# Kernel tuning notes

Measured on AMD Instinct MI355X. Metric: run time of the kernel, lower is better.

## Reference

```python
import jax, jax.numpy as jnp
import numpy as np
from jax import lax

B, L, NCH, NQ, NL, FW, NCLS = 256, 3000, 4, 8, 2, 128, 5
BN_EPS = 1e-5


def setup_inputs() -> dict:
    key = jax.random.key(0)
    ks = jax.random.split(key, 24)
    rn = lambda k, shape, s=0.05: jax.random.normal(k, shape, jnp.float32) * s
    inp = {}
    inp['x'] = jax.random.normal(ks[0], (B, NCH, L), jnp.float32)
    inp['conv1_w'] = rn(ks[1], (32, NCH, 7)); inp['conv1_b'] = rn(ks[2], (32,))
    inp['bn1_g'] = 1.0 + rn(ks[3], (32,)); inp['bn1_b'] = rn(ks[3], (32,))
    inp['conv2_w'] = rn(ks[4], (64, 32, 7)); inp['conv2_b'] = rn(ks[5], (64,))
    inp['bn2_g'] = 1.0 + rn(ks[6], (64,)); inp['bn2_b'] = rn(ks[6], (64,))
    inp['conv3_w'] = rn(ks[7], (128, 64, 7)); inp['conv3_b'] = rn(ks[8], (128,))
    inp['bn3_g'] = 1.0 + rn(ks[9], (128,)); inp['bn3_b'] = rn(ks[9], (128,))
    inp['conv4_w'] = rn(ks[10], (128, 128, 7)); inp['conv4_b'] = rn(ks[11], (128,))
    inp['bn4_g'] = 1.0 + rn(ks[12], (128,)); inp['bn4_b'] = rn(ks[12], (128,))
    inp['fc_w'] = rn(ks[13], (FW, 128)); inp['fc_b'] = rn(ks[14], (FW,))
    inp['ang_w'] = rn(ks[15], (NQ, FW)); inp['ang_b'] = rn(ks[16], (NQ,))
    # TorchLayer default init: uniform in [0, 2*pi)
    inp['qw'] = jax.random.uniform(ks[17], (NL, NQ, 3), jnp.float32, 0.0, 2.0 * np.pi)
    inp['h1_w'] = rn(ks[18], (64, NQ)); inp['h1_b'] = rn(ks[19], (64,))
    inp['h2_w'] = rn(ks[20], (NCLS, 64)); inp['h2_b'] = rn(ks[21], (NCLS,))
    return inp


def _conv1d(x, w, b):
    y = lax.conv_general_dilated(x, w, (1,), [(3, 3)], dimension_numbers=('NCH', 'OIH', 'NCH'))
    return y + b[None, :, None]


def _bn(x, g, b):  # eval-mode BN: running_mean=0, running_var=1
    inv = 1.0 / np.sqrt(1.0 + BN_EPS)
    return x * (g * inv)[None, :, None] + b[None, :, None]


def _maxpool4(x):
    return lax.reduce_window(x, -jnp.inf, lax.max, (1, 1, 4), (1, 1, 4), 'VALID')


def _apply_1q(state, U, w, batched):
    # state: (B, 2**NQ); wire 0 = most significant bit (PennyLane convention)
    bs = state.shape[0]
    st = state.reshape(bs, 2 ** w, 2, -1)
    if batched:
        new = jnp.einsum('sab,slbr->slar', U, st)
    else:
        new = jnp.einsum('ab,slbr->slar', U, st)
    return new.reshape(bs, -1)


def _apply_cnot(state, c, t):
    bs = state.shape[0]
    q1, q2 = min(c, t), max(c, t)
    s = state.reshape(bs, 2 ** q1, 2, 2 ** (q2 - q1 - 1), 2, -1)
    ci, ti = (2, 4) if c < t else (4, 2)
    c0 = lax.index_in_dim(s, 0, ci, keepdims=True)
    c1 = jnp.flip(lax.index_in_dim(s, 1, ci, keepdims=True), axis=ti)
    return jnp.concatenate([c0, c1], axis=ci).reshape(bs, -1)


def _rot_matrix(phi, th, om):
    # PennyLane Rot(phi, theta, omega) = RZ(omega) RY(theta) RZ(phi)
    cm, sm = jnp.cos(th / 2), jnp.sin(th / 2)
    m00 = jnp.exp(-0.5j * (phi + om)) * cm
    m01 = -jnp.exp(0.5j * (phi - om)) * sm
    m10 = jnp.exp(-0.5j * (phi - om)) * sm
    m11 = jnp.exp(0.5j * (phi + om)) * cm
    return jnp.stack([jnp.stack([m00, m01]), jnp.stack([m10, m11])]).astype(jnp.complex64)


def _qsim(angles, qw):
    bs = angles.shape[0]
    dim = 2 ** NQ
    state = jnp.zeros((bs, dim), jnp.complex64).at[:, 0].set(1.0)
    # AngleEmbedding: RY(angle_w) on each wire (batched matrices)
    c, s = jnp.cos(angles / 2), jnp.sin(angles / 2)
    for w in range(NQ):
        U = jnp.stack([jnp.stack([c[:, w], -s[:, w]], -1),
                       jnp.stack([s[:, w], c[:, w]], -1)], -2).astype(jnp.complex64)
        state = _apply_1q(state, U, w, batched=True)
    # StronglyEntanglingLayers: Rot on each wire, then CNOT ring with range r
    for l in range(NL):
        for w in range(NQ):
            U = _rot_matrix(qw[l, w, 0], qw[l, w, 1], qw[l, w, 2])
            state = _apply_1q(state, U, w, batched=False)
        r = (l % (NQ - 1)) + 1
        for i in range(NQ):
            state = _apply_cnot(state, i, (i + r) % NQ)
    probs = state.real ** 2 + state.imag ** 2
    z = [probs.reshape(bs, 2 ** w, 2, -1)[:, :, 0].sum((1, 2))
         - probs.reshape(bs, 2 ** w, 2, -1)[:, :, 1].sum((1, 2)) for w in range(NQ)]
    return jnp.stack(z, -1)  # (B, NQ)


def reference(x, conv1_w, conv1_b, bn1_g, bn1_b, conv2_w, conv2_b, bn2_g, bn2_b,
              conv3_w, conv3_b, bn3_g, bn3_b, conv4_w, conv4_b, bn4_g, bn4_b,
              fc_w, fc_b, ang_w, ang_b, qw, h1_w, h1_b, h2_w, h2_b):
    h = jax.nn.relu(_bn(_conv1d(x, conv1_w, conv1_b), bn1_g, bn1_b))
    h = jax.nn.relu(_bn(_conv1d(h, conv2_w, conv2_b), bn2_g, bn2_b))
    h = _maxpool4(h)
    h = jax.nn.relu(_bn(_conv1d(h, conv3_w, conv3_b), bn3_g, bn3_b))
    h = _maxpool4(h)
    h = jax.nn.relu(_bn(_conv1d(h, conv4_w, conv4_b), bn4_g, bn4_b))
    h = h.mean(-1)  # AdaptiveAvgPool1d(1) + Flatten -> (B, 128)
    h = jax.nn.relu(h @ fc_w.T + fc_b)  # Dropout is identity in eval
    raw = h @ ang_w.T + ang_b
    angles = np.pi * jnp.tanh(raw)
    q = _qsim(angles, qw)
    h2 = jax.nn.relu(q @ h1_w.T + h1_b)
    return h2 @ h2_w.T + h2_b
```

## Files before the change

### kernel.cpp

```cpp
#include <hip/hip_runtime.h>
#include <hip/hip_bf16.h>

#define BN_INV 0.9999950000375f
#define PI_F   3.14159265358979f

typedef __attribute__((ext_vector_type(8))) short s16x8;
typedef __attribute__((ext_vector_type(4))) float f32x4;
typedef __attribute__((ext_vector_type(4))) unsigned short u16x4;

__device__ inline unsigned short f2bf(float f) {
  union { float f; unsigned u; } v; v.f = f;
  unsigned r = v.u + 0x7fffu + ((v.u >> 16) & 1u);
  return (unsigned short)(r >> 16);
}

__global__ __launch_bounds__(256) void k_pack(
    const float* __restrict__ w1, const float* __restrict__ w2,
    const float* __restrict__ w3, const float* __restrict__ w4,
    unsigned short* __restrict__ w1p, unsigned short* __restrict__ w2p,
    unsigned short* __restrict__ w3p, unsigned short* __restrict__ w4p,
    float* __restrict__ h4)
{
  int e = blockIdx.x * 256 + threadIdx.x;
  if (e < 2048) {
    int co = e >> 6, k = e & 63, kk = k >> 3, ci = k & 7;
    w1p[e] = (ci < 4 && kk < 7) ? f2bf(w1[co * 28 + ci * 7 + kk]) : (unsigned short)0;
  } else if (e < 16384) {
    int t = e - 2048; int co = t / 224, k = t % 224, kk = k >> 5, ci = k & 31;
    w2p[t] = f2bf(w2[co * 224 + ci * 7 + kk]);
  } else if (e < 73728) {
    int t = e - 16384; int co = t / 448, k = t % 448, kk = k >> 6, ci = k & 63;
    w3p[t] = f2bf(w3[co * 448 + ci * 7 + kk]);
  } else if (e < 188416) {
    int t = e - 73728; int co = t / 896, k = t % 896, kk = k >> 7, ci = k & 127;
    w4p[t] = f2bf(w4[co * 896 + ci * 7 + kk]);
  } else if (e < 221184) {
    h4[e - 188416] = 0.f;
  }
}

__global__ __launch_bounds__(256) void k_conv1(
    const float* __restrict__ x, const unsigned short* __restrict__ w1p,
    const float* __restrict__ cb, const float* __restrict__ bng,
    const float* __restrict__ bnb, unsigned short* __restrict__ h1t)
{
  __shared__ __align__(16) char lds[520 * 16 + 4096 + 256];
  float* scs = (float*)(lds + 520 * 16 + 4096);
  const int tid = threadIdx.x;
  const int b = blockIdx.y;
  const int l0 = blockIdx.x * 512;

  for (int r = tid; r < 519; r += 256) {
    int gr = l0 + r - 3;
    s16x8 v;
    if (gr >= 0 && gr < 3000) {
      const float* xr = x + b * 4 * 3000 + gr;
      v[0] = (short)f2bf(xr[0]);
      v[1] = (short)f2bf(xr[3000]);
      v[2] = (short)f2bf(xr[6000]);
      v[3] = (short)f2bf(xr[9000]);
      v[4] = 0; v[5] = 0; v[6] = 0; v[7] = 0;
    } else {
      for (int i = 0; i < 8; ++i) v[i] = 0;
    }
    *(s16x8*)(lds + r * 16) = v;
  }
  {
    int co = tid >> 3, c = tid & 7;
    s16x8 v = *(const s16x8*)(w1p + co * 64 + c * 8);
    *(s16x8*)(lds + 8320 + ((co * 128 + c * 16) ^ ((co & 7) << 4))) = v;
  }
  if (tid < 32) {
    float sc = bng[tid] * BN_INV;
    scs[tid * 2] = sc;
    scs[tid * 2 + 1] = fmaf(cb[tid], sc, bnb[tid]);
  }
  __syncthreads();

  const int w = tid >> 6, l = tid & 63, lr = l & 15, g = l >> 4;
  const int wp = w * 128;
  f32x4 acc[2][8];
  for (int m = 0; m < 2; ++m)
    for (int n = 0; n < 8; ++n)
      for (int i = 0; i < 4; ++i) acc[m][n][i] = 0.f;

  #pragma unroll
  for (int s = 0; s < 2; ++s) {
    s16x8 a[2], bf[8];
    #pragma unroll
    for (int m = 0; m < 2; ++m) {
      int co = m * 16 + lr;
      a[m] = *(const s16x8*)(lds + 8320 + ((co * 128 + s * 64 + g * 16) ^ ((co & 7) << 4)));
    }
    #pragma unroll
    for (int n = 0; n < 8; ++n) {
      int row = wp + n * 16 + lr + s * 4 + g;
      bf[n] = *(const s16x8*)(lds + row * 16);
    }
    #pragma unroll
    for (int m = 0; m < 2; ++m)
      #pragma unroll
      for (int n = 0; n < 8; ++n)
        acc[m][n] = __builtin_amdgcn_mfma_f32_16x16x32_bf16(a[m], bf[n], acc[m][n], 0, 0, 0);
  }

  #pragma unroll
  for (int m = 0; m < 2; ++m) {
    int co0 = m * 16 + g * 4;
    float sc[4], sh[4];
    #pragma unroll
    for (int j = 0; j < 4; ++j) { sc[j] = scs[(co0 + j) * 2]; sh[j] = scs[(co0 + j) * 2 + 1]; }
    #pragma unroll
    for (int n = 0; n < 8; ++n) {
      int gp = l0 + wp + n * 16 + lr;
      if (gp < 3000) {
        u16x4 o;
        #pragma unroll
        for (int j = 0; j < 4; ++j)
          o[j] = f2bf(fmaxf(fmaf(acc[m][n][j], sc[j], sh[j]), 0.f));
        *(u16x4*)(h1t + (b * 3000 + gp) * 32 + co0) = o;
      }
    }
  }
}

__global__ __launch_bounds__(256) void k_conv2(
    const unsigned short* __restrict__ h1t, const unsigned short* __restrict__ w2p,
    const float* __restrict__ cb, const float* __restrict__ bng,
    const float* __restrict__ bnb, unsigned short* __restrict__ h2pt)
{
  __shared__ __align__(16) char lds[46080];
  float* scs = (float*)(lds + 45568);
  const int tid = threadIdx.x, b = blockIdx.y;
  const int l0 = blockIdx.x * 256;

  for (int e = tid; e < 1048; e += 256) {
    int r = e >> 2, c = e & 3;
    int gr = l0 + r - 3;
    s16x8 v;
    if (gr >= 0 && gr < 3000) v = *(const s16x8*)(h1t + (b * 3000 + gr) * 32 + c * 8);
    else for (int i = 0; i < 8; ++i) v[i] = 0;
    *(s16x8*)(lds + ((r * 64 + c * 16) ^ ((r & 7) << 4))) = v;
  }
  for (int e = tid; e < 1792; e += 256) {
    int co = e / 28, c = e % 28;
    s16x8 v = *(const s16x8*)(w2p + co * 224 + c * 8);
    *(s16x8*)(lds + 16896 + ((co * 448 + c * 16) ^ ((co & 7) << 4))) = v;
  }
  if (tid < 64) {
    float sc = bng[tid] * BN_INV;
    scs[tid * 2] = sc;
    scs[tid * 2 + 1] = fmaf(cb[tid], sc, bnb[tid]);
  }
  __syncthreads();

  const int w = tid >> 6, l = tid & 63, lr = l & 15, g = l >> 4;
  const int wp = w * 64;
  f32x4 acc[4][4];
  for (int m = 0; m < 4; ++m)
    for (int n = 0; n < 4; ++n)
      for (int i = 0; i < 4; ++i) acc[m][n][i] = 0.f;

  #pragma unroll
  for (int s = 0; s < 7; ++s) {
    s16x8 xa[4], wb[4];
    #pragma unroll
    for (int m = 0; m < 4; ++m) {
      int row = wp + m * 16 + lr + s;
      xa[m] = *(const s16x8*)(lds + ((row * 64 + g * 16) ^ ((row & 7) << 4)));
    }
    #pragma unroll
    for (int n = 0; n < 4; ++n) {
      int co = n * 16 + lr;
      wb[n] = *(const s16x8*)(lds + 16896 + ((co * 448 + s * 64 + g * 16) ^ ((co & 7) << 4)));
    }
    #pragma unroll
    for (int m = 0; m < 4; ++m)
      #pragma unroll
      for (int n = 0; n < 4; ++n)
        acc[m][n] = __builtin_amdgcn_mfma_f32_16x16x32_bf16(xa[m], wb[n], acc[m][n], 0, 0, 0);
  }

  float sc[4], sh[4];
  #pragma unroll
  for (int n = 0; n < 4; ++n) {
    sc[n] = scs[(n * 16 + lr) * 2];
    sh[n] = scs[(n * 16 + lr) * 2 + 1];
  }
  #pragma unroll
  for (int m = 0; m < 4; ++m) {
    int pp = (l0 + wp + m * 16 + g * 4) >> 2;
    if (pp < 750) {
      unsigned short* orow = h2pt + (b * 750 + pp) * 64 + lr;
      #pragma unroll
      for (int n = 0; n < 4; ++n) {
        float v = fmaxf(fmaxf(acc[m][n][0], acc[m][n][1]),
                        fmaxf(acc[m][n][2], acc[m][n][3]));
        orow[n * 16] = f2bf(fmaxf(fmaf(v, sc[n], sh[n]), 0.f));
      }
    }
  }
}

__global__ __launch_bounds__(256) void k_conv3(
    const unsigned short* __restrict__ h2pt, const unsigned short* __restrict__ w3p,
    const float* __restrict__ cb, const float* __restrict__ bng,
    const float* __restrict__ bnb, unsigned short* __restrict__ h3pt)
{
  __shared__ __align__(16) char lds[75776];
  float* scs = (float*)(lds + 74752);
  const int tid = threadIdx.x, b = blockIdx.y;
  const int tile = blockIdx.x >> 1, ch = blockIdx.x & 1;
  const int l0 = tile * 128, cg0 = ch * 64;

  for (int e = tid; e < 1072; e += 256) {
    int r = e >> 3, c = e & 7;
    int gr = l0 + r - 3;
    s16x8 v;
    if (gr >= 0 && gr < 750) v = *(const s16x8*)(h2pt + (b * 750 + gr) * 64 + c * 8);
    else for (int i = 0; i < 8; ++i) v[i] = 0;
    *(s16x8*)(lds + ((r * 128 + c * 16) ^ ((r & 7) << 4))) = v;
  }
  for (int e = tid; e < 3584; e += 256) {
    int co = e / 56, c = e % 56;
    s16x8 v = *(const s16x8*)(w3p + (cg0 + co) * 448 + c * 8);
    *(s16x8*)(lds + 17408 + ((co * 896 + c * 16) ^ ((co & 7) << 4))) = v;
  }
  if (tid < 64) {
    int co = cg0 + tid;
    float sc = bng[co] * BN_INV;
    scs[tid * 2] = sc;
    scs[tid * 2 + 1] = fmaf(cb[co], sc, bnb[co]);
  }
  __syncthreads();

  const int w = tid >> 6, l = tid & 63, lr = l & 15, g = l >> 4;
  const int wp = w * 32;
  f32x4 acc[2][4];
  for (int m = 0; m < 2; ++m)
    for (int n = 0; n < 4; ++n)
      for (int i = 0; i < 4; ++i) acc[m][n][i] = 0.f;

  #pragma unroll
  for (int sl = 0; sl < 14; ++sl) {
    int kk = sl >> 1, cib = (sl & 1) * 32;
    s16x8 xa[2], wb[4];
    #pragma unroll
    for (int m = 0; m < 2; ++m) {
      int row = wp + m * 16 + lr + kk;
      xa[m] = *(const s16x8*)(lds + ((row * 128 + cib * 2 + g * 16) ^ ((row & 7) << 4)));
    }
    #pragma unroll
    for (int n = 0; n < 4; ++n) {
      int co = n * 16 + lr;
      wb[n] = *(const s16x8*)(lds + 17408 + ((co * 896 + sl * 64 + g * 16) ^ ((co & 7) << 4)));
    }
    #pragma unroll
    for (int m = 0; m < 2; ++m)
      #pragma unroll
      for (int n = 0; n < 4; ++n)
        acc[m][n] = __builtin_amdgcn_mfma_f32_16x16x32_bf16(xa[m], wb[n], acc[m][n], 0, 0, 0);
  }

  float sc[4], sh[4];
  #pragma unroll
  for (int n = 0; n < 4; ++n) {
    sc[n] = scs[(n * 16 + lr) * 2];
    sh[n] = scs[(n * 16 + lr) * 2 + 1];
  }
  #pragma unroll
  for (int m = 0; m < 2; ++m) {
    int pp = (l0 + wp + m * 16 + g * 4) >> 2;
    if (pp < 187) {
      unsigned short* orow = h3pt + (b * 187 + pp) * 128 + cg0 + lr;
      #pragma unroll
      for (int n = 0; n < 4; ++n) {
        float v = fmaxf(fmaxf(acc[m][n][0], acc[m][n][1]),
                        fmaxf(acc[m][n][2], acc[m][n][3]));
        orow[n * 16] = f2bf(fmaxf(fmaf(v, sc[n], sh[n]), 0.f));
      }
    }
  }
}

__global__ __launch_bounds__(256) void k_conv4(
    const unsigned short* __restrict__ h3pt, const unsigned short* __restrict__ w4p,
    const float* __restrict__ cb, const float* __restrict__ bng,
    const float* __restrict__ bnb, float* __restrict__ h4)
{
  __shared__ __align__(16) char lds[79872];
  float* scs = (float*)(lds + 79360);
  const int tid = threadIdx.x, b = blockIdx.y, ch = blockIdx.x;
  const int cg0 = ch * 64;

  #pragma unroll
  for (int i = 0; i < 13; ++i) {
    int e = tid + i * 256;
    if (e < 3168) {
      int r = e >> 4, c = e & 15, gr = r - 3;
      s16x8 v;
      if (gr >= 0 && gr < 187) v = *(const s16x8*)(h3pt + (b * 187 + gr) * 128 + c * 8);
      else for (int q = 0; q < 8; ++q) v[q] = 0;
      *(s16x8*)(lds + ((r * 256 + c * 16) ^ ((r & 7) << 4))) = v;
    }
  }
  for (int e = tid; e < 1792; e += 256) {
    int co = e / 28, c = e % 28;
    s16x8 v = *(const s16x8*)(w4p + (cg0 + co) * 896 + c * 8);
    *(s16x8*)(lds + 50688 + ((co * 448 + c * 16) ^ ((co & 7) << 4))) = v;
  }
  if (tid < 64) {
    int co = cg0 + tid;
    float sc = bng[co] * BN_INV;
    scs[tid * 2] = sc;
    scs[tid * 2 + 1] = fmaf(cb[co], sc, bnb[co]);
  }
  __syncthreads();

  const int w = tid >> 6, l = tid & 63, lr = l & 15, g = l >> 4;
  const int wp = w * 48;

  f32x4 acc[3][4];
  for (int m = 0; m < 3; ++m)
    for (int n = 0; n < 4; ++n)
      for (int i = 0; i < 4; ++i) acc[m][n][i] = 0.f;

  for (int chunk = 0; chunk < 4; ++chunk) {
    s16x8 wr[7];
    if (chunk < 3) {
      #pragma unroll
      for (int i = 0; i < 7; ++i) {
        int e = tid + i * 256;
        int co = e / 28, c = e % 28;
        wr[i] = *(const s16x8*)(w4p + (cg0 + co) * 896 + (chunk + 1) * 224 + c * 8);
      }
    }
    #pragma unroll
    for (int sl = 0; sl < 7; ++sl) {
      int k0 = chunk * 224 + sl * 32;
      int kk = k0 >> 7, cib = k0 & 127;
      s16x8 xa[3], wb[4];
      #pragma unroll
      for (int m = 0; m < 3; ++m) {
        int row = wp + m * 16 + lr + kk;
        xa[m] = *(const s16x8*)(lds + ((row * 256 + cib * 2 + g * 16) ^ ((row & 7) << 4)));
      }
      #pragma unroll
      for (int n = 0; n < 4; ++n) {
        int co = n * 16 + lr;
        wb[n] = *(const s16x8*)(lds + 50688 + ((co * 448 + sl * 64 + g * 16) ^ ((co & 7) << 4)));
      }
      #pragma unroll
      for (int m = 0; m < 3; ++m)
        #pragma unroll
        for (int n = 0; n < 4; ++n)
          acc[m][n] = __builtin_amdgcn_mfma_f32_16x16x32_bf16(xa[m], wb[n], acc[m][n], 0, 0, 0);
    }
    __syncthreads();
    if (chunk < 3) {
      #pragma unroll
      for (int i = 0; i < 7; ++i) {
        int e = tid + i * 256;
        int co = e / 28, c = e % 28;
        *(s16x8*)(lds + 50688 + ((co * 448 + c * 16) ^ ((co & 7) << 4))) = wr[i];
      }
    }
    __syncthreads();
  }

  float sc[4], sh[4];
  #pragma unroll
  for (int n = 0; n < 4; ++n) {
    sc[n] = scs[(n * 16 + lr) * 2];
    sh[n] = scs[(n * 16 + lr) * 2 + 1];
  }
  float psum[4] = {0.f, 0.f, 0.f, 0.f};
  #pragma unroll
  for (int m = 0; m < 3; ++m) {
    #pragma unroll
    for (int j = 0; j < 4; ++j) {
      int pos = wp + m * 16 + g * 4 + j;
      if (pos < 187) {
        #pragma unroll
        for (int n = 0; n < 4; ++n)
          psum[n] += fmaxf(fmaf(acc[m][n][j], sc[n], sh[n]), 0.f);
      }
    }
  }
  #pragma unroll
  for (int n = 0; n < 4; ++n) {
    float v = psum[n];
    v += __shfl_xor(v, 16);
    v += __shfl_xor(v, 32);
    if (l < 16)
      atomicAdd(&h4[b * 128 + cg0 + n * 16 + lr], v);
  }
}

__global__ __launch_bounds__(64) void k_head(
    const float* __restrict__ h4, const float* __restrict__ fc_w,
    const float* __restrict__ fc_b, const float* __restrict__ ang_w,
    const float* __restrict__ ang_b, const float* __restrict__ qw,
    const float* __restrict__ h1_w, const float* __restrict__ h1_b,
    const float* __restrict__ h2_w, const float* __restrict__ h2_b,
    float* __restrict__ out)
{
  const int lane = threadIdx.x;
  const int b = blockIdx.x;

  float hv0 = h4[b * 128 + lane] * (1.0f / 187.0f);
  float hv1 = h4[b * 128 + 64 + lane] * (1.0f / 187.0f);

  float a0 = fc_b[lane], a1 = fc_b[lane + 64];
  {
    const float* w0 = fc_w + lane * 128;
    const float* w1 = fc_w + (lane + 64) * 128;
    #pragma unroll
    for (int k = 0; k < 64; ++k) {
      float hk = __shfl(hv0, k);
      a0 = fmaf(hk, w0[k], a0);
      a1 = fmaf(hk, w1[k], a1);
    }
    #pragma unroll
    for (int k = 0; k < 64; ++k) {
      float hk = __shfl(hv1, k);
      a0 = fmaf(hk, w0[64 + k], a0);
      a1 = fmaf(hk, w1[64 + k], a1);
    }
  }
  float f0 = fmaxf(a0, 0.f), f1 = fmaxf(a1, 0.f);

  float rcw[8], rsw[8];
  #pragma unroll
  for (int o = 0; o < 8; ++o) {
    float p = fmaf(f0, ang_w[o * 128 + lane], f1 * ang_w[o * 128 + 64 + lane]);
    #pragma unroll
    for (int m = 1; m < 64; m <<= 1) p += __shfl_xor(p, m);
    float aa = PI_F * tanhf(ang_b[o] + p);
    rcw[o] = cosf(0.5f * aa);
    rsw[o] = sinf(0.5f * aa);
  }

  float r0, r1, r2, r3, r4, r5, r6, r7;
  {
    int gq = lane & 15;
    float phi = qw[gq * 3], th = qw[gq * 3 + 1], om = qw[gq * 3 + 2];
    float cm = cosf(0.5f * th), sm = sinf(0.5f * th);
    float ap = 0.5f * (phi + om), bm = 0.5f * (phi - om);
    float ca = cosf(ap), sa = sinf(ap), cb2 = cosf(bm), sb2 = sinf(bm);
    r0 = cm * ca;   r1 = -cm * sa;
    r2 = -sm * cb2; r3 = -sm * sb2;
    r4 = sm * cb2;  r5 = -sm * sb2;
    r6 = cm * ca;   r7 = cm * sa;
  }

  float2 st[4];
  st[0] = make_float2((lane == 0) ? 1.f : 0.f, 0.f);
  st[1] = make_float2(0.f, 0.f);
  st[2] = make_float2(0.f, 0.f);
  st[3] = make_float2(0.f, 0.f);

  auto ry_lane = [&](int lx, float c, float s) {
    #pragma unroll
    for (int j = 0; j < 4; ++j) {
      float ox = __shfl_xor(st[j].x, lx);
      float oy = __shfl_xor(st[j].y, lx);
      bool hi = (lane & lx) != 0;
      float a0x = hi ? ox : st[j].x, a0y = hi ? oy : st[j].y;
      float a1x = hi ? st[j].x : ox, a1y = hi ? st[j].y : oy;
      float cA = hi ? s : c, cB = hi ? c : -s;
      st[j].x = cA * a0x + cB * a1x;
      st[j].y = cA * a0y + cB * a1y;
    }
  };
#define RY_SLOT(J0, J1, c, s) { \
    float2 A = st[J0], B = st[J1]; \
    st[J0].x = (c) * A.x - (s) * B.x; st[J0].y = (c) * A.y - (s) * B.y; \
    st[J1].x = (s) * A.x + (c) * B.x; st[J1].y = (s) * A.y + (c) * B.y; }

  ry_lane(32, rcw[0], rsw[0]);
  ry_lane(16, rcw[1], rsw[1]);
  ry_lane(8,  rcw[2], rsw[2]);
  ry_lane(4,  rcw[3], rsw[3]);
  ry_lane(2,  rcw[4], rsw[4]);
  ry_lane(1,  rcw[5], rsw[5]);
  RY_SLOT(0, 2, rcw[6], rsw[6]); RY_SLOT(1, 3, rcw[6], rsw[6]);
  RY_SLOT(0, 1, rcw[7], rsw[7]); RY_SLOT(2, 3, rcw[7], rsw[7]);

  auto rot_lane = [&](int gi, int lx) {
    float m00x = __shfl(r0, gi), m00y = __shfl(r1, gi);
    float m01x = __shfl(r2, gi), m01y = __shfl(r3, gi);
    float m10x = __shfl(r4, gi), m10y = __shfl(r5, gi);
    float m11x = __shfl(r6, gi), m11y = __shfl(r7, gi);
    #pragma unroll
    for (int j = 0; j < 4; ++j) {
      float ox = __shfl_xor(st[j].x, lx);
      float oy = __shfl_xor(st[j].y, lx);
      bool hi = (lane & lx) != 0;
      float a0x = hi ? ox : st[j].x, a0y = hi ? oy : st[j].y;
      float a1x = hi ? st[j].x : ox, a1y = hi ? st[j].y : oy;
      float cx = hi ? m10x : m00x, cy = hi ? m10y : m00y;
      float dx = hi ? m11x : m01x, dy = hi ? m11y : m01y;
      st[j].x = cx * a0x - cy * a0y + dx * a1x - dy * a1y;
      st[j].y = cx * a0y + cy * a0x + dx * a1y + dy * a1x;
    }
  };
#define ROT_SLOT(J0, J1) { \
    float2 A = st[J0], B = st[J1]; \
    st[J0].x = m00x * A.x - m00y * A.y + m01x * B.x - m01y * B.y; \
    st[J0].y = m00x * A.y + m00y * A.x + m01x * B.y + m01y * B.x; \
    st[J1].x = m10x * A.x - m10y * A.y + m11x * B.x - m11y * B.y; \
    st[J1].y = m10x * A.y + m10y * A.x + m11x * B.y + m11y * B.x; }
  auto rot_slot = [&](int gi, int bit) {
    float m00x = __shfl(r0, gi), m00y = __shfl(r1, gi);
    float m01x = __shfl(r2, gi), m01y = __shfl(r3, gi);
    float m10x = __shfl(r4, gi), m10y = __shfl(r5, gi);
    float m11x = __shfl(r6, gi), m11y = __shfl(r7, gi);
    if (bit == 1) { ROT_SLOT(0, 2) ROT_SLOT(1, 3) }
    else          { ROT_SLOT(0, 1) ROT_SLOT(2, 3) }
  };

  auto cnot = [&](int cmask, int tmask) {
    bool cb0, cb1, cb2, cb3;
    if (cmask >= 4) {
      bool cbl = (lane & (cmask >> 2)) != 0;
      cb0 = cbl; cb1 = cbl; cb2 = cbl; cb3 = cbl;
    } else {
      cb0 = false;
      cb1 = (1 & cmask) != 0;
      cb2 = (2 & cmask) != 0;
      cb3 = (3 & cmask) != 0;
    }
    if (tmask >= 4) {
      int lx = tmask >> 2;
      { float ox = __shfl_xor(st[0].x, lx), oy = __shfl_xor(st[0].y, lx); if (cb0) { st[0].x = ox; st[0].y = oy; } }
      { float ox = __shfl_xor(st[1].x, lx), oy = __shfl_xor(st[1].y, lx); if (cb1) { st[1].x = ox; st[1].y = oy; } }
      { float ox = __shfl_xor(st[2].x, lx), oy = __shfl_xor(st[2].y, lx); if (cb2) { st[2].x = ox; st[2].y = oy; } }
      { float ox = __shfl_xor(st[3].x, lx), oy = __shfl_xor(st[3].y, lx); if (cb3) { st[3].x = ox; st[3].y = oy; } }
    } else {
      float2 o0 = st[0], o1 = st[1], o2 = st[2], o3 = st[3];
      if (tmask == 2) {
        if (cb0) st[0] = o2;
        if (cb1) st[1] = o3;
        if (cb2) st[2] = o0;
        if (cb3) st[3] = o1;
      } else {
        if (cb0) st[0] = o1;
        if (cb1) st[1] = o0;
        if (cb2) st[2] = o3;
        if (cb3) st[3] = o2;
      }
    }
  };

  #pragma unroll
  for (int lay = 0; lay < 2; ++lay) {
    rot_lane(lay * 8 + 0, 32);
    rot_lane(lay * 8 + 1, 16);
    rot_lane(lay * 8 + 2, 8);
    rot_lane(lay * 8 + 3, 4);
    rot_lane(lay * 8 + 4, 2);
    rot_lane(lay * 8 + 5, 1);
    rot_slot(lay * 8 + 6, 1);
    rot_slot(lay * 8 + 7, 0);
    int r = lay + 1;
    #pragma unroll
    for (int i = 0; i < 8; ++i) {
      int c = i, t = (i + r) & 7;
      cnot(1 << (7 - c), 1 << (7 - t));
    }
  }

  float p0 = st[0].x * st[0].x + st[0].y * st[0].y;
  float p1 = st[1].x * st[1].x + st[1].y * st[1].y;
  float p2 = st[2].x * st[2].x + st[2].y * st[2].y;
  float p3 = st[3].x * st[3].x + st[3].y * st[3].y;
  float sAll = p0 + p1 + p2 + p3;
  float zp[8];
  zp[0] = (lane & 32) ? -sAll : sAll;
  zp[1] = (lane & 16) ? -sAll : sAll;
  zp[2] = (lane & 8)  ? -sAll : sAll;
  zp[3] = (lane & 4)  ? -sAll : sAll;
  zp[4] = (lane & 2)  ? -sAll : sAll;
  zp[5] = (lane & 1)  ? -sAll : sAll;
  zp[6] = (p0 + p1) - (p2 + p3);
  zp[7] = (p0 - p1) + (p2 - p3);
  #pragma unroll
  for (int o = 0; o < 8; ++o) {
    #pragma unroll
    for (int m = 1; m < 64; m <<= 1) zp[o] += __shfl_xor(zp[o], m);
  }

  float ah = h1_b[lane];
  const float* hw = h1_w + lane * 8;
  #pragma unroll
  for (int k = 0; k < 8; ++k) ah = fmaf(zp[k], hw[k], ah);
  float hh = fmaxf(ah, 0.f);

  #pragma unroll
  for (int o = 0; o < 5; ++o) {
    float v = hh * h2_w[o * 64 + lane];
    #pragma unroll
    for (int m = 1; m < 64; m <<= 1) v += __shfl_xor(v, m);
    if (lane == 0) out[b * 5 + o] = v + h2_b[o];
  }
#undef RY_SLOT
#undef ROT_SLOT
}

extern "C" void kernel_launch(void* const* d_in, const int* in_sizes, int n_in,
                              void* d_out, int out_size, void* d_ws, size_t ws_size,
                              hipStream_t stream) {
  (void)in_sizes; (void)n_in; (void)out_size; (void)ws_size;
  const float* x    = (const float*)d_in[0];
  const float* c1w  = (const float*)d_in[1];
  const float* c1b  = (const float*)d_in[2];
  const float* b1g  = (const float*)d_in[3];
  const float* b1b  = (const float*)d_in[4];
  const float* c2w  = (const float*)d_in[5];
  const float* c2b  = (const float*)d_in[6];
  const float* b2g  = (const float*)d_in[7];
  const float* b2b  = (const float*)d_in[8];
  const float* c3w  = (const float*)d_in[9];
  const float* c3b  = (const float*)d_in[10];
  const float* b3g  = (const float*)d_in[11];
  const float* b3b  = (const float*)d_in[12];
  const float* c4w  = (const float*)d_in[13];
  const float* c4b  = (const float*)d_in[14];
  const float* b4g  = (const float*)d_in[15];
  const float* b4b  = (const float*)d_in[16];
  const float* fcw  = (const float*)d_in[17];
  const float* fcb  = (const float*)d_in[18];
  const float* angw = (const float*)d_in[19];
  const float* angb = (const float*)d_in[20];
  const float* qw   = (const float*)d_in[21];
  const float* h1w  = (const float*)d_in[22];
  const float* h1b  = (const float*)d_in[23];
  const float* h2w  = (const float*)d_in[24];
  const float* h2b  = (const float*)d_in[25];

  char* wsb = (char*)d_ws;
  unsigned short* w1p  = (unsigned short*)(wsb + 0);
  unsigned short* w2p  = (unsigned short*)(wsb + 4096);
  unsigned short* w3p  = (unsigned short*)(wsb + 32768);
  unsigned short* w4p  = (unsigned short*)(wsb + 147456);
  float*          h4   = (float*)(wsb + 393216);
  unsigned short* h1t  = (unsigned short*)(wsb + 1048576);
  unsigned short* h2pt = (unsigned short*)(wsb + 52428800);
  unsigned short* h3pt = (unsigned short*)(wsb + 79691776);

  k_pack<<<dim3(864), 256, 0, stream>>>(c1w, c2w, c3w, c4w, w1p, w2p, w3p, w4p, h4);
  k_conv1<<<dim3(6, 256),  256, 0, stream>>>(x, w1p, c1b, b1g, b1b, h1t);
  k_conv2<<<dim3(12, 256), 256, 0, stream>>>(h1t, w2p, c2b, b2g, b2b, h2pt);
  k_conv3<<<dim3(12, 256), 256, 0, stream>>>(h2pt, w3p, c3b, b3g, b3b, h3pt);
  k_conv4<<<dim3(2, 256),  256, 0, stream>>>(h3pt, w4p, c4b, b4g, b4b, h4);
  k_head<<<dim3(256), 64, 0, stream>>>(h4, fcw, fcb, angw, angb, qw,
                                       h1w, h1b, h2w, h2b, (float*)d_out);
}
```

Measured before the change: 229.6 us.

## Precompute quantum circuit unitary, batch head, and widen conv3 tiles

Adds a kernel that builds the full 256x256 complex unitary of the fixed variational circuit from qw. The head then applies it to the product-state input, which is formed from per-sample RY cos/sin products, with a small matrix-vector product per sample instead of simulating gates per sample. The head also processes four samples per block and uses a transposed fc weight that the pack kernel prepares. Separately, conv3 now computes all 128 output channels per block over a 128-position tile, double-staging weights through registers, which halves the grid and avoids loading the input tile twice; the larger accumulator raises register pressure.

```diff
diff --git a/kernel.cpp b/kernel.cpp
--- a/kernel.cpp
+++ b/kernel.cpp
@@ -17,9 +17,10 @@
 __global__ __launch_bounds__(256) void k_pack(
     const float* __restrict__ w1, const float* __restrict__ w2,
     const float* __restrict__ w3, const float* __restrict__ w4,
+    const float* __restrict__ fcw,
     unsigned short* __restrict__ w1p, unsigned short* __restrict__ w2p,
     unsigned short* __restrict__ w3p, unsigned short* __restrict__ w4p,
-    float* __restrict__ h4)
+    float* __restrict__ fcwt, float* __restrict__ h4)
 {
   int e = blockIdx.x * 256 + threadIdx.x;
   if (e < 2048) {
@@ -36,6 +37,9 @@
     w4p[t] = f2bf(w4[co * 896 + ci * 7 + kk]);
   } else if (e < 221184) {
     h4[e - 188416] = 0.f;
+  } else if (e < 237568) {
+    int t = e - 221184; int k = t >> 7, o = t & 127;
+    fcwt[t] = fcw[o * 128 + k];
   }
 }
 
@@ -210,8 +214,7 @@
   __shared__ __align__(16) char lds[75776];
   float* scs = (float*)(lds + 74752);
   const int tid = threadIdx.x, b = blockIdx.y;
-  const int tile = blockIdx.x >> 1, ch = blockIdx.x & 1;
-  const int l0 = tile * 128, cg0 = ch * 64;
+  const int l0 = blockIdx.x * 128;
 
   for (int e = tid; e < 1072; e += 256) {
     int r = e >> 3, c = e & 7;
@@ -222,62 +225,86 @@
     *(s16x8*)(lds + ((r * 128 + c * 16) ^ ((r & 7) << 4))) = v;
   }
   for (int e = tid; e < 3584; e += 256) {
-    int co = e / 56, c = e % 56;
-    s16x8 v = *(const s16x8*)(w3p + (cg0 + co) * 448 + c * 8);
-    *(s16x8*)(lds + 17408 + ((co * 896 + c * 16) ^ ((co & 7) << 4))) = v;
-  }
-  if (tid < 64) {
-    int co = cg0 + tid;
-    float sc = bng[co] * BN_INV;
+    int co = e / 28, c = e % 28;
+    s16x8 v = *(const s16x8*)(w3p + co * 448 + c * 8);
+    *(s16x8*)(lds + 17408 + ((co * 448 + c * 16) ^ ((co & 7) << 4))) = v;
+  }
+  if (tid < 128) {
+    float sc = bng[tid] * BN_INV;
     scs[tid * 2] = sc;
-    scs[tid * 2 + 1] = fmaf(cb[co], sc, bnb[co]);
-  }
-  __syncthreads();
-
-  const int w = tid >> 6, l = tid & 63, lr = l & 15, g = l >> 4;
-  const int wp = w * 32;
-  f32x4 acc[2][4];
-  for (int m = 0; m < 2; ++m)
+    scs[tid * 2 + 1] = fmaf(cb[tid], sc, bnb[tid]);
+  }
+
+  const int lane = tid & 63, wid = tid >> 6;
+  const int wr = wid >> 1, wc = wid & 1;
+  const int lr = lane & 15, g = lane >> 4;
+
+  f32x4 acc[4][4];
+  for (int m = 0; m < 4; ++m)
     for (int n = 0; n < 4; ++n)
       for (int i = 0; i < 4; ++i) acc[m][n][i] = 0.f;
 
-  #pragma unroll
-  for (int sl = 0; sl < 14; ++sl) {
-    int kk = sl >> 1, cib = (sl & 1) * 32;
-    s16x8 xa[2], wb[4];
-    #pragma unroll
-    for (int m = 0; m < 2; ++m) {
-      int row = wp + m * 16 + lr + kk;
-      xa[m] = *(const s16x8*)(lds + ((row * 128 + cib * 2 + g * 16) ^ ((row & 7) << 4)));
-    }
-    #pragma unroll
-    for (int n = 0; n < 4; ++n) {
-      int co = n * 16 + lr;
-      wb[n] = *(const s16x8*)(lds + 17408 + ((co * 896 + sl * 64 + g * 16) ^ ((co & 7) << 4)));
-    }
-    #pragma unroll
-    for (int m = 0; m < 2; ++m)
-      #pragma unroll
-      for (int n = 0; n < 4; ++n)
-        acc[m][n] = __builtin_amdgcn_mfma_f32_16x16x32_bf16(xa[m], wb[n], acc[m][n], 0, 0, 0);
+  s16x8 pw[14];
+  #pragma unroll
+  for (int i = 0; i < 14; ++i) {
+    int e = tid + i * 256;
+    int co = e / 28, c = e % 28;
+    pw[i] = *(const s16x8*)(w3p + co * 448 + 224 + c * 8);
+  }
+  __syncthreads();
+
+  for (int chunk = 0; chunk < 2; ++chunk) {
+    #pragma unroll
+    for (int sl = 0; sl < 7; ++sl) {
+      int k0 = chunk * 224 + sl * 32;
+      int kk = k0 >> 6, cib = k0 & 63;
+      s16x8 xa[4], wb[4];
+      #pragma unroll
+      for (int m = 0; m < 4; ++m) {
+        int row = wr * 64 + m * 16 + lr + kk;
+        xa[m] = *(const s16x8*)(lds + ((row * 128 + cib * 2 + g * 16) ^ ((row & 7) << 4)));
+      }
+      #pragma unroll
+      for (int n = 0; n < 4; ++n) {
+        int co = wc * 64 + n * 16 + lr;
+        wb[n] = *(const s16x8*)(lds + 17408 + ((co * 448 + sl * 64 + g * 16) ^ ((co & 7) << 4)));
+      }
+      #pragma unroll
+      for (int m = 0; m < 4; ++m)
+        #pragma unroll
+        for (int n = 0; n < 4; ++n)
+          acc[m][n] = __builtin_amdgcn_mfma_f32_16x16x32_bf16(xa[m], wb[n], acc[m][n], 0, 0, 0);
+    }
+    if (chunk == 0) {
+      __syncthreads();
+      #pragma unroll
+      for (int i = 0; i < 14; ++i) {
+        int e = tid + i * 256;
+        int co = e / 28, c = e % 28;
+        *(s16x8*)(lds + 17408 + ((co * 448 + c * 16) ^ ((co & 7) << 4))) = pw[i];
+      }
+      __syncthreads();
+    }
   }
 
   float sc[4], sh[4];
   #pragma unroll
   for (int n = 0; n < 4; ++n) {
-    sc[n] = scs[(n * 16 + lr) * 2];
-    sh[n] = scs[(n * 16 + lr) * 2 + 1];
-  }
-  #pragma unroll
-  for (int m = 0; m < 2; ++m) {
-    int pp = (l0 + wp + m * 16 + g * 4) >> 2;
+    int co = wc * 64 + n * 16 + lr;
+    sc[n] = scs[co * 2];
+    sh[n] = scs[co * 2 + 1];
+  }
+  #pragma unroll
+  for (int m = 0; m < 4; ++m) {
+    int pp = (l0 + wr * 64 + m * 16 + g * 4) >> 2;
     if (pp < 187) {
-      unsigned short* orow = h3pt + (b * 187 + pp) * 128 + cg0 + lr;
+      unsigned short* orow = h3pt + (b * 187 + pp) * 128;
       #pragma unroll
       for (int n = 0; n < 4; ++n) {
+        int co = wc * 64 + n * 16 + lr;
         float v = fmaxf(fmaxf(acc[m][n][0], acc[m][n][1]),
                         fmaxf(acc[m][n][2], acc[m][n][3]));
-        orow[n * 16] = f2bf(fmaxf(fmaf(v, sc[n], sh[n]), 0.f));
+        orow[co] = f2bf(fmaxf(fmaf(v, sc[n], sh[n]), 0.f));
       }
     }
   }
@@ -397,215 +424,228 @@
   }
 }
 
-__global__ __launch_bounds__(64) void k_head(
-    const float* __restrict__ h4, const float* __restrict__ fc_w,
-    const float* __restrict__ fc_b, const float* __restrict__ ang_w,
-    const float* __restrict__ ang_b, const float* __restrict__ qw,
-    const float* __restrict__ h1_w, const float* __restrict__ h1_b,
-    const float* __restrict__ h2_w, const float* __restrict__ h2_b,
-    float* __restrict__ out)
+__global__ __launch_bounds__(256) void k_umat(
+    const float* __restrict__ qw, float2* __restrict__ Ut)
 {
-  const int lane = threadIdx.x;
-  const int b = blockIdx.x;
-
-  float hv0 = h4[b * 128 + lane] * (1.0f / 187.0f);
-  float hv1 = h4[b * 128 + 64 + lane] * (1.0f / 187.0f);
-
-  float a0 = fc_b[lane], a1 = fc_b[lane + 64];
-  {
-    const float* w0 = fc_w + lane * 128;
-    const float* w1 = fc_w + (lane + 64) * 128;
-    #pragma unroll
-    for (int k = 0; k < 64; ++k) {
-      float hk = __shfl(hv0, k);
-      a0 = fmaf(hk, w0[k], a0);
-      a1 = fmaf(hk, w1[k], a1);
-    }
-    #pragma unroll
-    for (int k = 0; k < 64; ++k) {
-      float hk = __shfl(hv1, k);
-      a0 = fmaf(hk, w0[64 + k], a0);
-      a1 = fmaf(hk, w1[64 + k], a1);
-    }
-  }
-  float f0 = fmaxf(a0, 0.f), f1 = fmaxf(a1, 0.f);
-
-  float rcw[8], rsw[8];
-  #pragma unroll
-  for (int o = 0; o < 8; ++o) {
-    float p = fmaf(f0, ang_w[o * 128 + lane], f1 * ang_w[o * 128 + 64 + lane]);
-    #pragma unroll
-    for (int m = 1; m < 64; m <<= 1) p += __shfl_xor(p, m);
-    float aa = PI_F * tanhf(ang_b[o] + p);
-    rcw[o] = cosf(0.5f * aa);
-    rsw[o] = sinf(0.5f * aa);
-  }
-
-  float r0, r1, r2, r3, r4, r5, r6, r7;
-  {
-    int gq = lane & 15;
+  __shared__ float rotm[16][8];
+  const int tid = threadIdx.x;
+  if (tid < 16) {
+    int gq = tid;
     float phi = qw[gq * 3], th = qw[gq * 3 + 1], om = qw[gq * 3 + 2];
     float cm = cosf(0.5f * th), sm = sinf(0.5f * th);
     float ap = 0.5f * (phi + om), bm = 0.5f * (phi - om);
-    float ca = cosf(ap), sa = sinf(ap), cb2 = cosf(bm), sb2 = sinf(bm);
-    r0 = cm * ca;   r1 = -cm * sa;
-    r2 = -sm * cb2; r3 = -sm * sb2;
-    r4 = sm * cb2;  r5 = -sm * sb2;
-    r6 = cm * ca;   r7 = cm * sa;
-  }
-
-  float2 st[4];
-  st[0] = make_float2((lane == 0) ? 1.f : 0.f, 0.f);
-  st[1] = make_float2(0.f, 0.f);
-  st[2] = make_float2(0.f, 0.f);
-  st[3] = make_float2(0.f, 0.f);
-
-  auto ry_lane = [&](int lx, float c, float s) {
-    #pragma unroll
-    for (int j = 0; j < 4; ++j) {
-      float ox = __shfl_xor(st[j].x, lx);
-      float oy = __shfl_xor(st[j].y, lx);
-      bool hi = (lane & lx) != 0;
-      float a0x = hi ? ox : st[j].x, a0y = hi ? oy : st[j].y;
-      float a1x = hi ? st[j].x : ox, a1y = hi ? st[j].y : oy;
-      float cA = hi ? s : c, cB = hi ? c : -s;
-      st[j].x = cA * a0x + cB * a1x;
-      st[j].y = cA * a0y + cB * a1y;
-    }
-  };
-#define RY_SLOT(J0, J1, c, s) { \
-    float2 A = st[J0], B = st[J1]; \
-    st[J0].x = (c) * A.x - (s) * B.x; st[J0].y = (c) * A.y - (s) * B.y; \
-    st[J1].x = (s) * A.x + (c) * B.x; st[J1].y = (s) * A.y + (c) * B.y; }
-
-  ry_lane(32, rcw[0], rsw[0]);
-  ry_lane(16, rcw[1], rsw[1]);
-  ry_lane(8,  rcw[2], rsw[2]);
-  ry_lane(4,  rcw[3], rsw[3]);
-  ry_lane(2,  rcw[4], rsw[4]);
-  ry_lane(1,  rcw[5], rsw[5]);
-  RY_SLOT(0, 2, rcw[6], rsw[6]); RY_SLOT(1, 3, rcw[6], rsw[6]);
-  RY_SLOT(0, 1, rcw[7], rsw[7]); RY_SLOT(2, 3, rcw[7], rsw[7]);
-
-  auto rot_lane = [&](int gi, int lx) {
-    float m00x = __shfl(r0, gi), m00y = __shfl(r1, gi);
-    float m01x = __shfl(r2, gi), m01y = __shfl(r3, gi);
-    float m10x = __shfl(r4, gi), m10y = __shfl(r5, gi);
-    float m11x = __shfl(r6, gi), m11y = __shfl(r7, gi);
-    #pragma unroll
-    for (int j = 0; j < 4; ++j) {
-      float ox = __shfl_xor(st[j].x, lx);
-      float oy = __shfl_xor(st[j].y, lx);
-      bool hi = (lane & lx) != 0;
-      float a0x = hi ? ox : st[j].x, a0y = hi ? oy : st[j].y;
-      float a1x = hi ? st[j].x : ox, a1y = hi ? st[j].y : oy;
-      float cx = hi ? m10x : m00x, cy = hi ? m10y : m00y;
-      float dx = hi ? m11x : m01x, dy = hi ? m11y : m01y;
-      st[j].x = cx * a0x - cy * a0y + dx * a1x - dy * a1y;
-      st[j].y = cx * a0y + cy * a0x + dx * a1y + dy * a1x;
-    }
-  };
-#define ROT_SLOT(J0, J1) { \
-    float2 A = st[J0], B = st[J1]; \
-    st[J0].x = m00x * A.x - m00y * A.y + m01x * B.x - m01y * B.y; \
-    st[J0].y = m00x * A.y + m00y * A.x + m01x * B.y + m01y * B.x; \
-    st[J1].x = m10x * A.x - m10y * A.y + m11x * B.x - m11y * B.y; \
-    st[J1].y = m10x * A.y + m10y * A.x + m11x * B.y + m11y * B.x; }
-  auto rot_slot = [&](int gi, int bit) {
-    float m00x = __shfl(r0, gi), m00y = __shfl(r1, gi);
-    float m01x = __shfl(r2, gi), m01y = __shfl(r3, gi);
-    float m10x = __shfl(r4, gi), m10y = __shfl(r5, gi);
-    float m11x = __shfl(r6, gi), m11y = __shfl(r7, gi);
-    if (bit == 1) { ROT_SLOT(0, 2) ROT_SLOT(1, 3) }
-    else          { ROT_SLOT(0, 1) ROT_SLOT(2, 3) }
-  };
-
-  auto cnot = [&](int cmask, int tmask) {
-    bool cb0, cb1, cb2, cb3;
-    if (cmask >= 4) {
-      bool cbl = (lane & (cmask >> 2)) != 0;
-      cb0 = cbl; cb1 = cbl; cb2 = cbl; cb3 = cbl;
-    } else {
-      cb0 = false;
-      cb1 = (1 & cmask) != 0;
-      cb2 = (2 & cmask) != 0;
-      cb3 = (3 & cmask) != 0;
-    }
-    if (tmask >= 4) {
-      int lx = tmask >> 2;
-      { float ox = __shfl_xor(st[0].x, lx), oy = __shfl_xor(st[0].y, lx); if (cb0) { st[0].x = ox; st[0].y = oy; } }
-      { float ox = __shfl_xor(st[1].x, lx), oy = __shfl_xor(st[1].y, lx); if (cb1) { st[1].x = ox; st[1].y = oy; } }
-      { float ox = __shfl_xor(st[2].x, lx), oy = __shfl_xor(st[2].y, lx); if (cb2) { st[2].x = ox; st[2].y = oy; } }
-      { float ox = __shfl_xor(st[3].x, lx), oy = __shfl_xor(st[3].y, lx); if (cb3) { st[3].x = ox; st[3].y = oy; } }
-    } else {
-      float2 o0 = st[0], o1 = st[1], o2 = st[2], o3 = st[3];
-      if (tmask == 2) {
-        if (cb0) st[0] = o2;
-        if (cb1) st[1] = o3;
-        if (cb2) st[2] = o0;
-        if (cb3) st[3] = o1;
-      } else {
-        if (cb0) st[0] = o1;
-        if (cb1) st[1] = o0;
-        if (cb2) st[2] = o3;
-        if (cb3) st[3] = o2;
-      }
-    }
-  };
-
-  #pragma unroll
-  for (int lay = 0; lay < 2; ++lay) {
-    rot_lane(lay * 8 + 0, 32);
-    rot_lane(lay * 8 + 1, 16);
-    rot_lane(lay * 8 + 2, 8);
-    rot_lane(lay * 8 + 3, 4);
-    rot_lane(lay * 8 + 4, 2);
-    rot_lane(lay * 8 + 5, 1);
-    rot_slot(lay * 8 + 6, 1);
-    rot_slot(lay * 8 + 7, 0);
-    int r = lay + 1;
-    #pragma unroll
-    for (int i = 0; i < 8; ++i) {
-      int c = i, t = (i + r) & 7;
-      cnot(1 << (7 - c), 1 << (7 - t));
-    }
-  }
-
-  float p0 = st[0].x * st[0].x + st[0].y * st[0].y;
-  float p1 = st[1].x * st[1].x + st[1].y * st[1].y;
-  float p2 = st[2].x * st[2].x + st[2].y * st[2].y;
-  float p3 = st[3].x * st[3].x + st[3].y * st[3].y;
-  float sAll = p0 + p1 + p2 + p3;
-  float zp[8];
-  zp[0] = (lane & 32) ? -sAll : sAll;
-  zp[1] = (lane & 16) ? -sAll : sAll;
-  zp[2] = (lane & 8)  ? -sAll : sAll;
-  zp[3] = (lane & 4)  ? -sAll : sAll;
-  zp[4] = (lane & 2)  ? -sAll : sAll;
-  zp[5] = (lane & 1)  ? -sAll : sAll;
-  zp[6] = (p0 + p1) - (p2 + p3);
-  zp[7] = (p0 - p1) + (p2 - p3);
-  #pragma unroll
-  for (int o = 0; o < 8; ++o) {
-    #pragma unroll
-    for (int m = 1; m < 64; m <<= 1) zp[o] += __shfl_xor(zp[o], m);
-  }
-
-  float ah = h1_b[lane];
-  const float* hw = h1_w + lane * 8;
-  #pragma unroll
-  for (int k = 0; k < 8; ++k) ah = fmaf(zp[k], hw[k], ah);
-  float hh = fmaxf(ah, 0.f);
-
-  #pragma unroll
-  for (int o = 0; o < 5; ++o) {
-    float v = hh * h2_w[o * 64 + lane];
-    #pragma unroll
-    for (int m = 1; m < 64; m <<= 1) v += __shfl_xor(v, m);
-    if (lane == 0) out[b * 5 + o] = v + h2_b[o];
-  }
-#undef RY_SLOT
-#undef ROT_SLOT
+    rotm[gq][0] = cm * cosf(ap);  rotm[gq][1] = -cm * sinf(ap);
+    rotm[gq][2] = -sm * cosf(bm); rotm[gq][3] = -sm * sinf(bm);
+    rotm[gq][4] = sm * cosf(bm);  rotm[gq][5] = -sm * sinf(bm);
+    rotm[gq][6] = cm * cosf(ap);  rotm[gq][7] = cm * sinf(ap);
+  }
+  __syncthreads();
+
+  const int lane = tid & 63, wid = tid >> 6;
+  const int ll = lane & 15;
+  const int c = (blockIdx.x * 4 + wid) * 4 + (lane >> 4);
+
+  float2 st[16];
+  #pragma unroll
+  for (int r = 0; r < 16; ++r) {
+    st[r].x = (ll == (c >> 4) && r == (c & 15)) ? 1.f : 0.f;
+    st[r].y = 0.f;
+  }
+
+#define LOADM(G) \
+  float m00x = rotm[G][0], m00y = rotm[G][1], m01x = rotm[G][2], m01y = rotm[G][3], \
+        m10x = rotm[G][4], m10y = rotm[G][5], m11x = rotm[G][6], m11y = rotm[G][7];
+
+#define ROT_REG(G, BETA) { LOADM(G) \
+  _Pragma("unroll") \
+  for (int r = 0; r < 16; ++r) if (!(r & BETA)) { \
+    float2 A = st[r], B = st[r + BETA]; \
+    st[r].x = m00x*A.x - m00y*A.y + m01x*B.x - m01y*B.y; \
+    st[r].y = m00x*A.y + m00y*A.x + m01x*B.y + m01y*B.x; \
+    st[r+BETA].x = m10x*A.x - m10y*A.y + m11x*B.x - m11y*B.y; \
+    st[r+BETA].y = m10x*A.y + m10y*A.x + m11x*B.y + m11y*B.x; } }
+
+#define ROT_LANE(G, LX) { LOADM(G) \
+  _Pragma("unroll") \
+  for (int r = 0; r < 16; ++r) { \
+    float ox = __shfl_xor(st[r].x, LX); \
+    float oy = __shfl_xor(st[r].y, LX); \
+    bool hi = (lane & LX) != 0; \
+    float a0x = hi ? ox : st[r].x, a0y = hi ? oy : st[r].y; \
+    float a1x = hi ? st[r].x : ox, a1y = hi ? st[r].y : oy; \
+    float cx = hi ? m10x : m00x, cy = hi ? m10y : m00y; \
+    float dx = hi ? m11x : m01x, dy = hi ? m11y : m01y; \
+    st[r].x = cx*a0x - cy*a0y + dx*a1x - dy*a1y; \
+    st[r].y = cx*a0y + cy*a0x + dx*a1y + dy*a1x; } }
+
+#define CNOT_RR(BC, BT) { \
+  _Pragma("unroll") \
+  for (int r = 0; r < 16; ++r) if ((r & BC) && !(r & BT)) { \
+    float2 t_ = st[r]; st[r] = st[r + BT]; st[r + BT] = t_; } }
+
+#define CNOT_RL(BC, LXT) { \
+  _Pragma("unroll") \
+  for (int r = 0; r < 16; ++r) if (r & BC) { \
+    st[r].x = __shfl_xor(st[r].x, LXT); \
+    st[r].y = __shfl_xor(st[r].y, LXT); } }
+
+#define CNOT_LR(LXC, BT) { bool cc = (lane & LXC) != 0; \
+  _Pragma("unroll") \
+  for (int r = 0; r < 16; ++r) if (!(r & BT)) { \
+    float2 A = st[r], B = st[r + BT]; \
+    st[r].x = cc ? B.x : A.x;  st[r].y = cc ? B.y : A.y; \
+    st[r+BT].x = cc ? A.x : B.x;  st[r+BT].y = cc ? A.y : B.y; } }
+
+#define CNOT_LL(LXC, LXT) { bool cc = (lane & LXC) != 0; \
+  _Pragma("unroll") \
+  for (int r = 0; r < 16; ++r) { \
+    float ox = __shfl_xor(st[r].x, LXT); \
+    float oy = __shfl_xor(st[r].y, LXT); \
+    if (cc) { st[r].x = ox; st[r].y = oy; } } }
+
+  ROT_LANE(0, 8) ROT_LANE(1, 4) ROT_LANE(2, 2) ROT_LANE(3, 1)
+  ROT_REG(4, 8)  ROT_REG(5, 4)  ROT_REG(6, 2)  ROT_REG(7, 1)
+  CNOT_LL(8, 4) CNOT_LL(4, 2) CNOT_LL(2, 1) CNOT_LR(1, 8)
+  CNOT_RR(8, 4) CNOT_RR(4, 2) CNOT_RR(2, 1) CNOT_RL(1, 8)
+  ROT_LANE(8, 8) ROT_LANE(9, 4) ROT_LANE(10, 2) ROT_LANE(11, 1)
+  ROT_REG(12, 8) ROT_REG(13, 4) ROT_REG(14, 2)  ROT_REG(15, 1)
+  CNOT_LL(8, 2) CNOT_LL(4, 1) CNOT_LR(2, 8) CNOT_LR(1, 4)
+  CNOT_RR(8, 2) CNOT_RR(4, 1) CNOT_RL(2, 8) CNOT_RL(1, 4)
+
+#undef LOADM
+#undef ROT_REG
+#undef ROT_LANE
+#undef CNOT_RR
+#undef CNOT_RL
+#undef CNOT_LR
+#undef CNOT_LL
+
+  float2* uc = Ut + c * 256 + ll * 16;
+  #pragma unroll
+  for (int r = 0; r < 16; r += 2) {
+    float4 v = make_float4(st[r].x, st[r].y, st[r + 1].x, st[r + 1].y);
+    *(float4*)(uc + r) = v;
+  }
+}
+
+__global__ __launch_bounds__(256) void k_head2(
+    const float* __restrict__ h4, const float* __restrict__ fc_wt,
+    const float* __restrict__ fc_b, const float* __restrict__ ang_w,
+    const float* __restrict__ ang_b, const float* __restrict__ h1_w,
+    const float* __restrict__ h1_b, const float* __restrict__ h2_w,
+    const float* __restrict__ h2_b, const float2* __restrict__ Ut,
+    float* __restrict__ out)
+{
+  __shared__ float h4v[512];
+  __shared__ float fvec[512];
+  __shared__ float rcs[64];
+  __shared__ float4 e4[256];
+  __shared__ float4 parr[256];
+  __shared__ float zsum[32];
+  __shared__ float hh[256];
+
+  const int tid = threadIdx.x;
+  const int b0 = blockIdx.x * 4;
+
+  #pragma unroll
+  for (int q = 0; q < 2; ++q) {
+    int task = tid + q * 256;
+    h4v[task] = h4[(b0 + (task >> 7)) * 128 + (task & 127)] * (1.0f / 187.0f);
+  }
+  __syncthreads();
+
+  #pragma unroll
+  for (int q = 0; q < 2; ++q) {
+    int task = tid + q * 256;
+    int bb = task >> 7, o = task & 127;
+    float a = fc_b[o];
+    const float* hv = h4v + bb * 128;
+    #pragma unroll 8
+    for (int k = 0; k < 128; ++k) a = fmaf(hv[k], fc_wt[k * 128 + o], a);
+    fvec[task] = fmaxf(a, 0.f);
+  }
+  __syncthreads();
+
+  if (tid < 32) {
+    int bb = tid >> 3, o = tid & 7;
+    float a = ang_b[o];
+    const float* fv = fvec + bb * 128;
+    const float* wr = ang_w + o * 128;
+    for (int k = 0; k < 128; ++k) a = fmaf(fv[k], wr[k], a);
+    float ang = PI_F * tanhf(a);
+    rcs[bb * 16 + o * 2]     = cosf(0.5f * ang);
+    rcs[bb * 16 + o * 2 + 1] = sinf(0.5f * ang);
+  }
+  __syncthreads();
+
+  {
+    float4 ev;
+    #pragma unroll
+    for (int bb = 0; bb < 4; ++bb) {
+      float prod = 1.f;
+      #pragma unroll
+      for (int w = 0; w < 8; ++w) {
+        float cc = rcs[bb * 16 + w * 2];
+        float ss = rcs[bb * 16 + w * 2 + 1];
+        prod *= ((tid >> (7 - w)) & 1) ? ss : cc;
+      }
+      ev[bb] = prod;
+    }
+    e4[tid] = ev;
+  }
+  __syncthreads();
+
+  {
+    float ax0 = 0.f, ax1 = 0.f, ax2 = 0.f, ax3 = 0.f;
+    float ay0 = 0.f, ay1 = 0.f, ay2 = 0.f, ay3 = 0.f;
+    #pragma unroll 4
+    for (int cc = 0; cc < 256; ++cc) {
+      float2 u = Ut[cc * 256 + tid];
+      float4 ev = e4[cc];
+      ax0 = fmaf(u.x, ev[0], ax0); ay0 = fmaf(u.y, ev[0], ay0);
+      ax1 = fmaf(u.x, ev[1], ax1); ay1 = fmaf(u.y, ev[1], ay1);
+      ax2 = fmaf(u.x, ev[2], ax2); ay2 = fmaf(u.y, ev[2], ay2);
+      ax3 = fmaf(u.x, ev[3], ax3); ay3 = fmaf(u.y, ev[3], ay3);
+    }
+    parr[tid] = make_float4(ax0 * ax0 + ay0 * ay0, ax1 * ax1 + ay1 * ay1,
+                            ax2 * ax2 + ay2 * ay2, ax3 * ax3 + ay3 * ay3);
+  }
+  __syncthreads();
+
+  {
+    int task = tid >> 3, part = tid & 7;
+    int bb = task >> 3, wq = task & 7;
+    int bit = 7 - wq;
+    float s = 0.f;
+    #pragma unroll 8
+    for (int i = 0; i < 32; ++i) {
+      int row = i * 8 + part;
+      const float* pr = (const float*)&parr[row];
+      float p = pr[bb];
+      s = ((row >> bit) & 1) ? (s - p) : (s + p);
+    }
+    s += __shfl_xor(s, 1);
+    s += __shfl_xor(s, 2);
+    s += __shfl_xor(s, 4);
+    if (part == 0) zsum[task] = s;
+  }
+  __syncthreads();
+
+  {
+    int bb = tid >> 6, o = tid & 63;
+    float a = h1_b[o];
+    #pragma unroll
+    for (int k = 0; k < 8; ++k) a = fmaf(zsum[bb * 8 + k], h1_w[o * 8 + k], a);
+    hh[tid] = fmaxf(a, 0.f);
+  }
+  __syncthreads();
+
+  if (tid < 20) {
+    int bb = tid / 5, o = tid % 5;
+    float a = h2_b[o];
+    for (int j = 0; j < 64; ++j) a = fmaf(hh[bb * 64 + j], h2_w[o * 64 + j], a);
+    out[(b0 + bb) * 5 + o] = a;
+  }
 }
 
 extern "C" void kernel_launch(void* const* d_in, const int* in_sizes, int n_in,
@@ -648,12 +688,16 @@
   unsigned short* h1t  = (unsigned short*)(wsb + 1048576);
   unsigned short* h2pt = (unsigned short*)(wsb + 52428800);
   unsigned short* h3pt = (unsigned short*)(wsb + 79691776);
-
-  k_pack<<<dim3(864), 256, 0, stream>>>(c1w, c2w, c3w, c4w, w1p, w2p, w3p, w4p, h4);
+  float2*         Ut   = (float2*)(wsb + 100663296);
+  float*          fcwt = (float*)(wsb + 101187584);
+
+  k_pack<<<dim3(928), 256, 0, stream>>>(c1w, c2w, c3w, c4w, fcw,
+                                        w1p, w2p, w3p, w4p, fcwt, h4);
+  k_umat<<<dim3(16), 256, 0, stream>>>(qw, Ut);
   k_conv1<<<dim3(6, 256),  256, 0, stream>>>(x, w1p, c1b, b1g, b1b, h1t);
   k_conv2<<<dim3(12, 256), 256, 0, stream>>>(h1t, w2p, c2b, b2g, b2b, h2pt);
-  k_conv3<<<dim3(12, 256), 256, 0, stream>>>(h2pt, w3p, c3b, b3g, b3b, h3pt);
+  k_conv3<<<dim3(6, 256),  256, 0, stream>>>(h2pt, w3p, c3b, b3g, b3b, h3pt);
   k_conv4<<<dim3(2, 256),  256, 0, stream>>>(h3pt, w4p, c4b, b4g, b4b, h4);
-  k_head<<<dim3(256), 64, 0, stream>>>(h4, fcw, fcb, angw, angb, qw,
-                                       h1w, h1b, h2w, h2b, (float*)d_out);
-}
+  k_head2<<<dim3(64), 256, 0, stream>>>(h4, fcwt, fcb, angw, angb,
+                                        h1w, h1b, h2w, h2b, Ut, (float*)d_out);
+}
```

Result: slower. 248.0 us (+8.0%).
